# Optimization experiments

Measured on AMD Instinct MI355X. Metric: run time of the kernel, lower is better.

The kernel has to match this reference:

```python
import jax, jax.numpy as jnp
import numpy as np

N_SIDE = 64                 # imageSize
H = N_SIDE * N_SIDE         # num_pixels = hidden = 4096
B = 128                     # batch
ITERS = 12                  # layers (propagation iterations)


def _grid_adjacency():
    # generateFixedWeightMask_PredPrey: pixel j couples to pixel i iff j is in the
    # 3x3 neighborhood of i on the imageSize x imageSize grid (incl. self).
    idx = np.arange(H)
    r, c = idx // N_SIDE, idx % N_SIDE
    adj = (np.abs(r[:, None] - r[None, :]) <= 1) & (np.abs(c[:, None] - c[None, :]) <= 1)
    return adj.astype(np.float32)


def setup_inputs() -> dict:
    key = jax.random.key(0)
    k1, k2, k3, k4 = jax.random.split(key, 4)
    hiddenWeight = jnp.asarray(_grid_adjacency())          # [H,H] 0/1, masked ones
    X = jax.random.normal(k1, (B, H), dtype=jnp.float32)
    pred = jax.random.normal(k2, (B, H), dtype=jnp.float32)
    w = jax.random.normal(k3, (H, 1), dtype=jnp.float32)   # per-row hidden scale
    a = jax.random.normal(k4, (H, 1), dtype=jnp.float32)   # per-pixel input scale
    bias = jnp.ones((H, 1), dtype=jnp.float32)
    scalar = jnp.full((1,), 2.0, dtype=jnp.float32)
    return {"X": X, "pred": pred, "w": w, "a": a, "bias": bias,
            "scalar": scalar, "hiddenWeight": hiddenWeight, "dtype": 1}


def reference(X, pred, w, a, bias, scalar, hiddenWeight, dtype):
    # u_fix: clamp prey-markers (-1) to 0, constant across iterations
    u_fix = jnp.where(pred == -1.0, 0.0, pred)             # [B,H]
    # inputWeight is diag(1) (diagMask), so (a*inputWeight)@x == a*x per pixel.
    const = u_fix + bias[:, 0] + a[:, 0] * X               # [B,H], loop-invariant
    Wm = w * hiddenWeight                                  # row-scaled masked weights, loop-invariant
    u = pred
    for _ in range(ITERS):
        v = const + jnp.einsum('ij,bj->bi', Wm, u)         # [B,H]
        u = jnp.tanh(v * scalar)
    return u
```

## Files before the change

kernel.cpp:

```cpp
#include <hip/hip_runtime.h>


#define NS     64
#define HH     (NS * NS)
#define ITERS  12
#define PITCH  68
#define ROWS   (NS + 2)
#define GP     (ROWS * PITCH)
#define PRE    4
#define BUFSZ  (GP + PRE)

__device__ __forceinline__ float fast_rcp(float x) {
#if __has_builtin(__builtin_amdgcn_rcpf)
  return __builtin_amdgcn_rcpf(x);
#else
  return 1.0f / x;
#endif
}

__global__ __launch_bounds__(512, 1)
void prop_kernel(const float* __restrict__ X,
                 const float* __restrict__ pred,
                 const float* __restrict__ w,
                 const float* __restrict__ a,
                 const float* __restrict__ bias,
                 const float* __restrict__ scalar,
                 float* __restrict__ out)
{
  __shared__ __align__(16) float pool[2][BUFSZ];

  const int t   = threadIdx.x;
  const int b   = blockIdx.x;
  const int r   = t >> 3;
  const int c0  = (t & 7) << 3;
  const int pix = r * NS + c0;

  {
    float4 z = make_float4(0.f, 0.f, 0.f, 0.f);
    float4* p4 = (float4*)&pool[0][0];
    const int n4 = (2 * BUFSZ) / 4;
    for (int i = t; i < n4; i += 512) p4[i] = z;
  }

  const size_t gb = (size_t)b * HH + pix;
  const float4 x0  = *(const float4*)(X    + gb);
  const float4 x1  = *(const float4*)(X    + gb + 4);
  const float4 p0  = *(const float4*)(pred + gb);
  const float4 p1  = *(const float4*)(pred + gb + 4);
  const float4 w0  = *(const float4*)(w    + pix);
  const float4 w1  = *(const float4*)(w    + pix + 4);
  const float4 a0  = *(const float4*)(a    + pix);
  const float4 a1  = *(const float4*)(a    + pix + 4);
  const float4 bb0 = *(const float4*)(bias + pix);
  const float4 bb1 = *(const float4*)(bias + pix + 4);
  const float  sc  = scalar[0];

  const float pv[8] = {p0.x, p0.y, p0.z, p0.w, p1.x, p1.y, p1.z, p1.w};
  const float xv[8] = {x0.x, x0.y, x0.z, x0.w, x1.x, x1.y, x1.z, x1.w};
  const float av[8] = {a0.x, a0.y, a0.z, a0.w, a1.x, a1.y, a1.z, a1.w};
  const float bv[8] = {bb0.x, bb0.y, bb0.z, bb0.w, bb1.x, bb1.y, bb1.z, bb1.w};
  const float wr[8] = {w0.x, w0.y, w0.z, w0.w, w1.x, w1.y, w1.z, w1.w};

  float cst[8];
#pragma unroll
  for (int k = 0; k < 8; ++k) {
    const float uf = (pv[k] == -1.0f) ? 0.0f : pv[k];
    cst[k] = uf + bv[k] + av[k] * xv[k];
  }

  __syncthreads();

  float* ua = &pool[0][PRE];
  float* ub = &pool[1][PRE];
  {
    float* dst = ua + (r + 1) * PITCH + c0;
    *(float4*)dst       = p0;
    *(float4*)(dst + 4) = p1;
  }
  __syncthreads();

  float un[8];
  for (int it = 0; it < ITERS; ++it) {
    float s[8] = {0.f, 0.f, 0.f, 0.f, 0.f, 0.f, 0.f, 0.f};
#pragma unroll
    for (int dr = 0; dr < 3; ++dr) {
      const float* rowp = ua + (r + dr) * PITCH + c0;
      const float4 m0 = *(const float4*)rowp;
      const float4 m1 = *(const float4*)(rowp + 4);
      const float mL = rowp[-1];
      const float mR = rowp[8];
      s[0] += mL   + m0.x + m0.y;
      s[1] += m0.x + m0.y + m0.z;
      s[2] += m0.y + m0.z + m0.w;
      s[3] += m0.z + m0.w + m1.x;
      s[4] += m0.w + m1.x + m1.y;
      s[5] += m1.x + m1.y + m1.z;
      s[6] += m1.y + m1.z + m1.w;
      s[7] += m1.z + m1.w + mR;
    }
#pragma unroll
    for (int k = 0; k < 8; ++k) {
      const float v  = fmaf(wr[k], s[k], cst[k]);
      const float tt = v * sc;
      const float e  = __expf(-2.0f * fabsf(tt));
      const float th = (1.0f - e) * fast_rcp(1.0f + e);
      un[k] = copysignf(th, tt);
    }
    if (it + 1 < ITERS) {
      float* dst = ub + (r + 1) * PITCH + c0;
      *(float4*)dst       = make_float4(un[0], un[1], un[2], un[3]);
      *(float4*)(dst + 4) = make_float4(un[4], un[5], un[6], un[7]);
      float* tmp = ua; ua = ub; ub = tmp;
      __syncthreads();
    }
  }

  float* op = out + gb;
  *(float4*)op       = make_float4(un[0], un[1], un[2], un[3]);
  *(float4*)(op + 4) = make_float4(un[4], un[5], un[6], un[7]);
}

extern "C" void kernel_launch(void* const* d_in, const int* in_sizes, int n_in,
                              void* d_out, int out_size, void* d_ws, size_t ws_size,
                              hipStream_t stream) {
  const float* X    = (const float*)d_in[0];
  const float* pred = (const float*)d_in[1];
  const float* w    = (const float*)d_in[2];
  const float* a    = (const float*)d_in[3];
  const float* bias = (const float*)d_in[4];
  const float* scal = (const float*)d_in[5];
  float* out = (float*)d_out;
  const int B = in_sizes[0] / HH;
  prop_kernel<<<B, 512, 0, stream>>>(X, pred, w, a, bias, scal, out);
}
```

Before: 118.0 us.

## Use DPP lane shifts for horizontal stencil sums and share only partial sums

Each thread now owns a 2-row by 4-column tile, and each 16-lane group maps to one image row. Horizontal 3-tap sums are built in registers, with edge values taken from neighbouring lanes through DPP row shifts; bound_ctrl makes the values at the grid edges zero. Only the horizontal partial sums go through LDS, and each thread reads just the rows above and below, so there is one barrier per iteration and only the halo rows are zero-initialised. The tanh is also rewritten with exp2 and a pre-folded scalar. The price is reliance on DPP row semantics and a double-buffer scheme whose correctness depends on that single barrier.

```diff
diff --git a/kernel.cpp b/kernel.cpp
--- a/kernel.cpp
+++ b/kernel.cpp
@@ -4,18 +4,26 @@
 #define NS     64
 #define HH     (NS * NS)
 #define ITERS  12
-#define PITCH  68
-#define ROWS   (NS + 2)
-#define GP     (ROWS * PITCH)
-#define PRE    4
-#define BUFSZ  (GP + PRE)
+#define HP     64
+#define HROWS  (NS + 2)
 
-__device__ __forceinline__ float fast_rcp(float x) {
+#if __has_builtin(__builtin_amdgcn_exp2f)
+#define EXP2F(x) __builtin_amdgcn_exp2f(x)
+#else
+#define EXP2F(x) exp2f(x)
+#endif
+
 #if __has_builtin(__builtin_amdgcn_rcpf)
-  return __builtin_amdgcn_rcpf(x);
+#define RCPF(x) __builtin_amdgcn_rcpf(x)
 #else
-  return 1.0f / x;
+#define RCPF(x) (1.0f / (x))
 #endif
+
+__device__ __forceinline__ float dpp_left(float x) {
+  return __int_as_float(__builtin_amdgcn_mov_dpp(__float_as_int(x), 0x111, 0xf, 0xf, true));
+}
+__device__ __forceinline__ float dpp_right(float x) {
+  return __int_as_float(__builtin_amdgcn_mov_dpp(__float_as_int(x), 0x101, 0xf, 0xf, true));
 }
 
 __global__ __launch_bounds__(512, 1)
@@ -27,97 +35,96 @@
                  const float* __restrict__ scalar,
                  float* __restrict__ out)
 {
-  __shared__ __align__(16) float pool[2][BUFSZ];
+  __shared__ __align__(16) float hbuf[2][HROWS * HP];
 
-  const int t   = threadIdx.x;
-  const int b   = blockIdx.x;
-  const int r   = t >> 3;
-  const int c0  = (t & 7) << 3;
-  const int pix = r * NS + c0;
+  const int t  = threadIdx.x;
+  const int b  = blockIdx.x;
+  const int r2 = t >> 4;
+  const int c0 = (t & 15) << 2;
+  const int r0 = r2 << 1;
 
-  {
-    float4 z = make_float4(0.f, 0.f, 0.f, 0.f);
-    float4* p4 = (float4*)&pool[0][0];
-    const int n4 = (2 * BUFSZ) / 4;
-    for (int i = t; i < n4; i += 512) p4[i] = z;
+  if (t < 64) {
+    const int buf = t >> 5;
+    const int bot = (t >> 4) & 1;
+    float4* p = (float4*)(&hbuf[buf][bot ? (HROWS - 1) * HP : 0]);
+    p[t & 15] = make_float4(0.f, 0.f, 0.f, 0.f);
   }
 
-  const size_t gb = (size_t)b * HH + pix;
-  const float4 x0  = *(const float4*)(X    + gb);
-  const float4 x1  = *(const float4*)(X    + gb + 4);
-  const float4 p0  = *(const float4*)(pred + gb);
-  const float4 p1  = *(const float4*)(pred + gb + 4);
-  const float4 w0  = *(const float4*)(w    + pix);
-  const float4 w1  = *(const float4*)(w    + pix + 4);
-  const float4 a0  = *(const float4*)(a    + pix);
-  const float4 a1  = *(const float4*)(a    + pix + 4);
+  const int    pix = r0 * NS + c0;
+  const size_t g0  = (size_t)b * HH + pix;
+
+  const float4 px0 = *(const float4*)(pred + g0);
+  const float4 px1 = *(const float4*)(pred + g0 + NS);
+  const float4 xx0 = *(const float4*)(X    + g0);
+  const float4 xx1 = *(const float4*)(X    + g0 + NS);
+  const float4 ww0 = *(const float4*)(w    + pix);
+  const float4 ww1 = *(const float4*)(w    + pix + NS);
+  const float4 aa0 = *(const float4*)(a    + pix);
+  const float4 aa1 = *(const float4*)(a    + pix + NS);
   const float4 bb0 = *(const float4*)(bias + pix);
-  const float4 bb1 = *(const float4*)(bias + pix + 4);
-  const float  sc  = scalar[0];
+  const float4 bb1 = *(const float4*)(bias + pix + NS);
 
-  const float pv[8] = {p0.x, p0.y, p0.z, p0.w, p1.x, p1.y, p1.z, p1.w};
-  const float xv[8] = {x0.x, x0.y, x0.z, x0.w, x1.x, x1.y, x1.z, x1.w};
-  const float av[8] = {a0.x, a0.y, a0.z, a0.w, a1.x, a1.y, a1.z, a1.w};
+  const float sc  = scalar[0];
+  const float c2  = -2.885390082f * fabsf(sc);
+  const float ssg = (sc < 0.f) ? -1.f : 1.f;
+
+  float un[8] = {px0.x, px0.y, px0.z, px0.w, px1.x, px1.y, px1.z, px1.w};
+  const float xv[8] = {xx0.x, xx0.y, xx0.z, xx0.w, xx1.x, xx1.y, xx1.z, xx1.w};
+  const float av[8] = {aa0.x, aa0.y, aa0.z, aa0.w, aa1.x, aa1.y, aa1.z, aa1.w};
   const float bv[8] = {bb0.x, bb0.y, bb0.z, bb0.w, bb1.x, bb1.y, bb1.z, bb1.w};
-  const float wr[8] = {w0.x, w0.y, w0.z, w0.w, w1.x, w1.y, w1.z, w1.w};
+  const float wr[8] = {ww0.x, ww0.y, ww0.z, ww0.w, ww1.x, ww1.y, ww1.z, ww1.w};
 
   float cst[8];
 #pragma unroll
   for (int k = 0; k < 8; ++k) {
-    const float uf = (pv[k] == -1.0f) ? 0.0f : pv[k];
+    const float uf = (un[k] == -1.0f) ? 0.0f : un[k];
     cst[k] = uf + bv[k] + av[k] * xv[k];
   }
 
-  __syncthreads();
+  float* hcur = &hbuf[0][HP];
+  float* hnxt = &hbuf[1][HP];
+  const int myoff = r0 * HP + c0;
 
-  float* ua = &pool[0][PRE];
-  float* ub = &pool[1][PRE];
-  {
-    float* dst = ua + (r + 1) * PITCH + c0;
-    *(float4*)dst       = p0;
-    *(float4*)(dst + 4) = p1;
-  }
-  __syncthreads();
+  for (int it = 0; it < ITERS; ++it) {
+    float h[8];
+#pragma unroll
+    for (int rr = 0; rr < 2; ++rr) {
+      const int kb = rr * 4;
+      const float hL = dpp_left(un[kb + 3]);
+      const float hR = dpp_right(un[kb + 0]);
+      h[kb + 0] = hL        + un[kb + 0] + un[kb + 1];
+      h[kb + 1] = un[kb + 0] + un[kb + 1] + un[kb + 2];
+      h[kb + 2] = un[kb + 1] + un[kb + 2] + un[kb + 3];
+      h[kb + 3] = un[kb + 2] + un[kb + 3] + hR;
+    }
+    *(float4*)(hcur + myoff)      = make_float4(h[0], h[1], h[2], h[3]);
+    *(float4*)(hcur + myoff + HP) = make_float4(h[4], h[5], h[6], h[7]);
+    __syncthreads();
 
-  float un[8];
-  for (int it = 0; it < ITERS; ++it) {
-    float s[8] = {0.f, 0.f, 0.f, 0.f, 0.f, 0.f, 0.f, 0.f};
+    const float4 mu = *(const float4*)(hcur + myoff - HP);
+    const float4 md = *(const float4*)(hcur + myoff + 2 * HP);
+    const float sU[4] = {mu.x, mu.y, mu.z, mu.w};
+    const float sD[4] = {md.x, md.y, md.z, md.w};
+
 #pragma unroll
-    for (int dr = 0; dr < 3; ++dr) {
-      const float* rowp = ua + (r + dr) * PITCH + c0;
-      const float4 m0 = *(const float4*)rowp;
-      const float4 m1 = *(const float4*)(rowp + 4);
-      const float mL = rowp[-1];
-      const float mR = rowp[8];
-      s[0] += mL   + m0.x + m0.y;
-      s[1] += m0.x + m0.y + m0.z;
-      s[2] += m0.y + m0.z + m0.w;
-      s[3] += m0.z + m0.w + m1.x;
-      s[4] += m0.w + m1.x + m1.y;
-      s[5] += m1.x + m1.y + m1.z;
-      s[6] += m1.y + m1.z + m1.w;
-      s[7] += m1.z + m1.w + mR;
+    for (int k = 0; k < 4; ++k) {
+      const float s0 = sU[k] + h[k] + h[4 + k];
+      const float s1 = h[k] + h[4 + k] + sD[k];
+      const float v0 = fmaf(wr[k],     s0, cst[k]);
+      const float v1 = fmaf(wr[4 + k], s1, cst[4 + k]);
+      const float e0 = EXP2F(c2 * fabsf(v0));
+      const float e1 = EXP2F(c2 * fabsf(v1));
+      const float t0 = (1.f - e0) * RCPF(1.f + e0);
+      const float t1 = (1.f - e1) * RCPF(1.f + e1);
+      un[k]     = ssg * copysignf(t0, v0);
+      un[4 + k] = ssg * copysignf(t1, v1);
     }
-#pragma unroll
-    for (int k = 0; k < 8; ++k) {
-      const float v  = fmaf(wr[k], s[k], cst[k]);
-      const float tt = v * sc;
-      const float e  = __expf(-2.0f * fabsf(tt));
-      const float th = (1.0f - e) * fast_rcp(1.0f + e);
-      un[k] = copysignf(th, tt);
-    }
-    if (it + 1 < ITERS) {
-      float* dst = ub + (r + 1) * PITCH + c0;
-      *(float4*)dst       = make_float4(un[0], un[1], un[2], un[3]);
-      *(float4*)(dst + 4) = make_float4(un[4], un[5], un[6], un[7]);
-      float* tmp = ua; ua = ub; ub = tmp;
-      __syncthreads();
-    }
+    float* tmp = hcur; hcur = hnxt; hnxt = tmp;
   }
 
-  float* op = out + gb;
-  *(float4*)op       = make_float4(un[0], un[1], un[2], un[3]);
-  *(float4*)(op + 4) = make_float4(un[4], un[5], un[6], un[7]);
+  float* op = out + g0;
+  *(float4*)op        = make_float4(un[0], un[1], un[2], un[3]);
+  *(float4*)(op + NS) = make_float4(un[4], un[5], un[6], un[7]);
 }
 
 extern "C" void kernel_launch(void* const* d_in, const int* in_sizes, int n_in,
```

New measurement: 109.0 us. 1.08x faster.
